# Kernel optimization log

Hardware: AMD Instinct MI355X
Metric: run time of the kernel (lower is better)

The kernel has to match this reference:

```python
import jax, jax.numpy as jnp
import numpy as np


def _lin(x, w, b):
    # torch Linear: y = x @ w.T + b, w shape [out, in]
    return x @ w.T + b


def setup_inputs() -> dict:
    key = jax.random.key(0)
    ks = jax.random.split(key, 24)
    D, L1, L2, L3, C = 784, 128, 64, 32, 10
    B = 65536
    s = 0.05
    inp = {
        'x': jax.random.normal(ks[0], (B, D), jnp.float32),
        'W1_w': jax.random.normal(ks[1], (L1, D), jnp.float32) * s,
        'W1_b': jnp.zeros((L1,), jnp.float32),
        'U1_w': jax.random.normal(ks[2], (L1, L1), jnp.float32) * s,
        'U1_b': jnp.zeros((L1,), jnp.float32),
        'W2_w': jax.random.normal(ks[3], (L2, L1), jnp.float32) * s,
        'W2_b': jnp.zeros((L2,), jnp.float32),
        'U2_w': jax.random.normal(ks[4], (L2, L2), jnp.float32) * s,
        'U2_b': jnp.zeros((L2,), jnp.float32),
        'W3_w': jax.random.normal(ks[5], (L3, L2), jnp.float32) * s,
        'W3_b': jnp.zeros((L3,), jnp.float32),
        'U3_w': jax.random.normal(ks[6], (L3, L3), jnp.float32) * s,
        'U3_b': jnp.zeros((L3,), jnp.float32),
        'fb3_w': jax.random.normal(ks[7], (L2, L3), jnp.float32) * s,
        'fb3_b': jnp.zeros((L2,), jnp.float32),
        'fb2_w': jax.random.normal(ks[8], (L1, L2), jnp.float32) * s,
        'fb2_b': jnp.zeros((L1,), jnp.float32),
        'fb1_w': jax.random.normal(ks[9], (D, L1), jnp.float32) * s,
        'fb1_b': jnp.zeros((D,), jnp.float32),
        'clf_w': jax.random.normal(ks[10], (C, L3), jnp.float32) * s,
        'clf_b': jnp.zeros((C,), jnp.float32),
        'steps': 5,
    }
    return inp


def reference(x, W1_w, W1_b, U1_w, U1_b, W2_w, W2_b, U2_w, U2_b,
              W3_w, W3_b, U3_w, U3_b, fb3_w, fb3_b, fb2_w, fb2_b,
              fb1_w, fb1_b, clf_w, clf_b, steps):
    B = x.shape[0]
    x = x.reshape(B, -1)
    h1 = jnp.zeros((B, W1_w.shape[0]), x.dtype)
    h2 = jnp.zeros((B, W2_w.shape[0]), x.dtype)
    h3 = jnp.zeros((B, W3_w.shape[0]), x.dtype)
    for _ in range(steps):  # fixed small step count (5)
        err_h2 = h2 - _lin(h3, fb3_w, fb3_b)
        err_h1 = h1 - _lin(h2, fb2_w, fb2_b)
        err_x = x - _lin(h1, fb1_w, fb1_b)
        h3 = h3 + jnp.tanh(_lin(err_h2, W3_w, W3_b)) + jnp.tanh(_lin(h3, U3_w, U3_b))
        h2 = h2 + jnp.tanh(_lin(err_h1, W2_w, W2_b)) + jnp.tanh(_lin(h2, U2_w, U2_b))
        h1 = h1 + jnp.tanh(_lin(err_x, W1_w, W1_b)) + jnp.tanh(_lin(h1, U1_w, U1_b))
    return _lin(h3, clf_w, clf_b)
```

## Files before the change

### kernel.cpp

```cpp
#include <hip/hip_runtime.h>
#include <stdint.h>

typedef __attribute__((ext_vector_type(8))) __bf16 bf16x8;
typedef __attribute__((ext_vector_type(8))) unsigned short u16x8;
typedef __attribute__((ext_vector_type(4))) unsigned short u16x4;
typedef __attribute__((ext_vector_type(4))) float f32x4;

#define WSF_M1 0
#define WSF_M2 16384
#define WSF_M3 20480
#define WSF_C  21504
#define F_W1T 0
#define F_M1N 102400
#define F_U1T 118784
#define F_W2T 135168
#define F_M2N 143360
#define F_U2T 147456
#define F_W3T 151552
#define F_M3N 153600
#define F_U3T 154624
#define F_CLF 155648

__device__ __forceinline__ unsigned short f2bf(float f) {
  uint32_t u = __builtin_bit_cast(uint32_t, f);
  u += 0x7fffu + ((u >> 16) & 1u);
  return (unsigned short)(u >> 16);
}

extern "C" __device__ float __ocml_native_exp2_f32(float);
__device__ __forceinline__ float tanh_fast(float x) {
  float e = __ocml_native_exp2_f32(x * 2.8853900817779268f);
  return 1.0f - 2.0f * __builtin_amdgcn_rcpf(e + 1.0f);
}

__device__ __forceinline__ f32x4 mfma16(bf16x8 a, bf16x8 b, f32x4 c) {
  return __builtin_amdgcn_mfma_f32_16x16x32_bf16(a, b, c, 0, 0, 0);
}

__device__ __forceinline__ bf16x8 lds_frag(const unsigned short* p) {
  u16x8 v = *(const u16x8*)p;
  return __builtin_bit_cast(bf16x8, v);
}
__device__ __forceinline__ bf16x8 glb_frag(const unsigned short* __restrict__ base,
                                           int fi, int lane) {
  u16x8 v = *(const u16x8*)(base + (((size_t)fi * 64 + lane) << 3));
  return __builtin_bit_cast(bf16x8, v);
}

__global__ __launch_bounds__(256)
void pcnet_prep(
    const float* __restrict__ W1_w, const float* __restrict__ W1_b,
    const float* __restrict__ W2_w, const float* __restrict__ W2_b,
    const float* __restrict__ W3_w, const float* __restrict__ W3_b,
    const float* __restrict__ fb1_w, const float* __restrict__ fb1_b,
    const float* __restrict__ fb2_w, const float* __restrict__ fb2_b,
    const float* __restrict__ fb3_w, const float* __restrict__ fb3_b,
    float* __restrict__ wsf)
{
  const int w    = blockIdx.x * 4 + (threadIdx.x >> 6);
  const int lane = threadIdx.x & 63;
  float s = 0.f;
  if (w < 16384) {
    const int a = w >> 7, b = w & 127;
    for (int d = lane; d < 784; d += 64) s += fb1_w[d*128 + a] * W1_w[b*784 + d];
  } else if (w < 20480) {
    const int t = w - 16384, a = t >> 6, b = t & 63;
    for (int d = lane; d < 128; d += 64) s += fb2_w[d*64 + a] * W2_w[b*128 + d];
  } else if (w < 21504) {
    const int t = w - 20480, a = t >> 5, b = t & 31;
    s = fb3_w[lane*32 + a] * W3_w[b*64 + lane];
  } else if (w < 21632) {
    const int b = w - 21504;
    for (int d = lane; d < 784; d += 64) s += fb1_b[d] * W1_w[b*784 + d];
  } else if (w < 21696) {
    const int b = w - 21632;
    for (int d = lane; d < 128; d += 64) s += fb2_b[d] * W2_w[b*128 + d];
  } else if (w < 21728) {
    const int b = w - 21696;
    s = fb3_b[lane] * W3_w[b*64 + lane];
  }
#pragma unroll
  for (int off = 32; off >= 1; off >>= 1) s += __shfl_down(s, off, 64);
  if (lane == 0) {
    if (w < 16384)      wsf[WSF_M1 + (w >> 7)*128 + (w & 127)] = -s;
    else if (w < 20480) { const int t = w - 16384; wsf[WSF_M2 + (t >> 6)*64 + (t & 63)] = -s; }
    else if (w < 21504) { const int t = w - 20480; wsf[WSF_M3 + (t >> 5)*32 + (t & 31)] = -s; }
    else if (w < 21632) { const int b = w - 21504; wsf[WSF_C + b]       = W1_b[b] - s; }
    else if (w < 21696) { const int b = w - 21632; wsf[WSF_C + 128 + b] = W2_b[b] - s; }
    else if (w < 21728) { const int b = w - 21696; wsf[WSF_C + 192 + b] = W3_b[b] - s; }
  }
}

__device__ __forceinline__ void swz_T(const float* __restrict__ src, int ld, int Kv, int Nv,
                                      int NT, unsigned short* __restrict__ dst, int f, int lane) {
  const int kt = f / NT, nt = f - kt*NT;
  const int m = lane & 15, q = lane >> 4;
  const int n = nt*16 + m;
  u16x8 v;
#pragma unroll
  for (int j = 0; j < 8; ++j) {
    const int k = kt*32 + q*8 + j;
    float val = (k < Kv && n < Nv) ? src[(size_t)n*ld + k] : 0.f;
    v[j] = f2bf(val);
  }
  *(u16x8*)(dst + (((size_t)f*64 + lane) << 3)) = v;
}
__device__ __forceinline__ void swz_R(const float* __restrict__ src, int N, int NT,
                                      unsigned short* __restrict__ dst, int f, int lane) {
  const int kt = f / NT, nt = f - kt*NT;
  const int m = lane & 15, q = lane >> 4;
  const int n = nt*16 + m;
  u16x8 v;
#pragma unroll
  for (int j = 0; j < 8; ++j) {
    const int k = kt*32 + q*8 + j;
    v[j] = f2bf(src[k*N + n]);
  }
  *(u16x8*)(dst + (((size_t)f*64 + lane) << 3)) = v;
}

__global__ void pcnet_swz(
    const float* __restrict__ W1_w, const float* __restrict__ U1_w,
    const float* __restrict__ W2_w, const float* __restrict__ U2_w,
    const float* __restrict__ W3_w, const float* __restrict__ U3_w,
    const float* __restrict__ clf_w, const float* __restrict__ wsf,
    unsigned short* __restrict__ frags)
{
  const int t = blockIdx.x*256 + threadIdx.x;
  if (t >= 305*64) return;
  const int fg = t >> 6, lane = t & 63;
  if      (fg < 200) swz_T(W1_w, 784, 784, 128, 8, frags + F_W1T, fg,       lane);
  else if (fg < 232) swz_R(wsf + WSF_M1, 128, 8,  frags + F_M1N, fg - 200, lane);
  else if (fg < 264) swz_T(U1_w, 128, 128, 128, 8, frags + F_U1T, fg - 232, lane);
  else if (fg < 280) swz_T(W2_w, 128, 128, 64, 4, frags + F_W2T, fg - 264, lane);
  else if (fg < 288) swz_R(wsf + WSF_M2, 64, 4,   frags + F_M2N, fg - 280, lane);
  else if (fg < 296) swz_T(U2_w, 64, 64, 64, 4,   frags + F_U2T, fg - 288, lane);
  else if (fg < 300) swz_T(W3_w, 64, 64, 32, 2,   frags + F_W3T, fg - 296, lane);
  else if (fg < 302) swz_R(wsf + WSF_M3, 32, 2,   frags + F_M3N, fg - 300, lane);
  else if (fg < 304) swz_T(U3_w, 32, 32, 32, 2,   frags + F_U3T, fg - 302, lane);
  else               swz_T(clf_w, 32, 32, 10, 1,  frags + F_CLF, fg - 304, lane);
}

__global__ __launch_bounds__(256, 2)
void pcnet_main(
    const float* __restrict__ x,
    const float* __restrict__ cvec,
    const float* __restrict__ U1_b, const float* __restrict__ U2_b,
    const float* __restrict__ U3_b, const float* __restrict__ clf_b,
    const unsigned short* __restrict__ frags,
    const int* __restrict__ steps_p,
    float* __restrict__ out)
{
  const int tid  = threadIdx.x;
  const int wave = tid >> 6;
  const int lane = tid & 63;
  const int q = lane >> 4;
  const int m = lane & 15;
  const int rowBase = blockIdx.x << 5;

  __shared__ unsigned short h1b[32*136];
  __shared__ unsigned short h2b[32*72];
  __shared__ unsigned short h3b[32*40];
  __shared__ unsigned short xst[2][32*40];

  const unsigned short* fW1T = frags + F_W1T;
  const unsigned short* fM1N = frags + F_M1N;
  const unsigned short* fU1T = frags + F_U1T;
  const unsigned short* fW2T = frags + F_W2T;
  const unsigned short* fM2N = frags + F_M2N;
  const unsigned short* fU2T = frags + F_U2T;
  const unsigned short* fW3T = frags + F_W3T;
  const unsigned short* fM3N = frags + F_M3N;
  const unsigned short* fU3T = frags + F_U3T;
  const unsigned short* fCLF = frags + F_CLF;

  f32x4 A1[2][2];
#pragma unroll
  for (int nt = 0; nt < 2; ++nt) {
    const float cv = cvec[(2*wave + nt)*16 + m];
    const f32x4 v = {cv, cv, cv, cv};
    A1[0][nt] = v; A1[1][nt] = v;
  }

  const int srow = tid >> 3;
  const int kq   = (tid & 7) << 2;
  const float* __restrict__ xrow = x + (size_t)(rowBase + srow)*784;

  {
    f32x4 va = *(const f32x4*)(xrow + kq);
    u16x4 pk;
    pk[0]=f2bf(va[0]); pk[1]=f2bf(va[1]); pk[2]=f2bf(va[2]); pk[3]=f2bf(va[3]);
    *(u16x4*)(xst[0] + srow*40 + kq) = pk;
  }

  for (int kt = 0; kt < 25; ++kt) {
    __syncthreads();
    if (kt < 24) {
      const int gk = (kt + 1)*32 + kq;
      f32x4 va = {0.f,0.f,0.f,0.f};
      if (gk < 784) va = *(const f32x4*)(xrow + gk);
      u16x4 pk;
      pk[0]=f2bf(va[0]); pk[1]=f2bf(va[1]); pk[2]=f2bf(va[2]); pk[3]=f2bf(va[3]);
      *(u16x4*)(xst[(kt+1)&1] + srow*40 + kq) = pk;
    }
    const unsigned short* xb = xst[kt & 1];
    const bf16x8 a0 = lds_frag(xb + (0*16 + m)*40 + q*8);
    const bf16x8 a1 = lds_frag(xb + (1*16 + m)*40 + q*8);
#pragma unroll
    for (int nt = 0; nt < 2; ++nt) {
      const bf16x8 b = glb_frag(fW1T, kt*8 + 2*wave + nt, lane);
      A1[0][nt] = mfma16(a0, b, A1[0][nt]);
      A1[1][nt] = mfma16(a1, b, A1[1][nt]);
    }
  }

  {
    uint32_t* p = (uint32_t*)h1b;
    for (int i = tid; i < 2176; i += 256) p[i] = 0u;
    p = (uint32_t*)h2b;
    for (int i = tid; i < 1152; i += 256) p[i] = 0u;
    p = (uint32_t*)h3b;
    for (int i = tid; i < 640; i += 256) p[i] = 0u;
  }
  f32x4 h1v[2][2], h2v[2], h3v;
  {
    const f32x4 z = {0.f,0.f,0.f,0.f};
#pragma unroll
    for (int rt = 0; rt < 2; ++rt) { h1v[rt][0] = z; h1v[rt][1] = z; h2v[rt] = z; }
    h3v = z;
  }

  const int nt3 = wave >> 1;
  const int rt3 = wave & 1;
  const float c3v  = cvec[192 + nt3*16 + m];
  const float b3v  = U3_b[nt3*16 + m];
  const float c2v  = cvec[128 + wave*16 + m];
  const float b2v  = U2_b[wave*16 + m];
  const float b1v0 = U1_b[(2*wave + 0)*16 + m];
  const float b1v1 = U1_b[(2*wave + 1)*16 + m];

  __syncthreads();

  const int S = *steps_p;
  for (int s = 0; s < S; ++s) {
    bf16x8 h2f[2][2];
#pragma unroll
    for (int kt = 0; kt < 2; ++kt)
#pragma unroll
      for (int rt = 0; rt < 2; ++rt)
        h2f[kt][rt] = lds_frag(h2b + (rt*16 + m)*72 + kt*32 + q*8);
    const bf16x8 h3f = lds_frag(h3b + (rt3*16 + m)*40 + q*8);
    bf16x8 h2s[2];
#pragma unroll
    for (int kt = 0; kt < 2; ++kt) h2s[kt] = (wave & 1) ? h2f[kt][1] : h2f[kt][0];

    f32x4 z3a = {c3v,c3v,c3v,c3v};
    f32x4 z3b = {b3v,b3v,b3v,b3v};
#pragma unroll
    for (int kt = 0; kt < 2; ++kt) {
      const bf16x8 b = glb_frag(fW3T, kt*2 + nt3, lane);
      z3a = mfma16(h2s[kt], b, z3a);
    }
    { const bf16x8 b = glb_frag(fM3N, nt3, lane); z3a = mfma16(h3f, b, z3a); }
    { const bf16x8 b = glb_frag(fU3T, nt3, lane); z3b = mfma16(h3f, b, z3b); }
#pragma unroll
    for (int r = 0; r < 4; ++r)
      h3v[r] += tanh_fast(z3a[r]) + tanh_fast(z3b[r]);

    f32x4 z2b[2];
    { const f32x4 v = {b2v,b2v,b2v,b2v}; z2b[0]=v; z2b[1]=v; }
#pragma unroll
    for (int kt = 0; kt < 2; ++kt) {
      const bf16x8 b = glb_frag(fU2T, kt*4 + wave, lane);
#pragma unroll
      for (int rt = 0; rt < 2; ++rt) z2b[rt] = mfma16(h2f[kt][rt], b, z2b[rt]);
    }
#pragma unroll
    for (int rt = 0; rt < 2; ++rt)
#pragma unroll
      for (int r = 0; r < 4; ++r) h2v[rt][r] += tanh_fast(z2b[rt][r]);

    f32x4 z2a[2];
    { const f32x4 v = {c2v,c2v,c2v,c2v}; z2a[0]=v; z2a[1]=v; }
#pragma unroll
    for (int kt = 0; kt < 2; ++kt) {
      const bf16x8 b = glb_frag(fM2N, kt*4 + wave, lane);
#pragma unroll
      for (int rt = 0; rt < 2; ++rt) z2a[rt] = mfma16(h2f[kt][rt], b, z2a[rt]);
    }

    f32x4 z1a[2][2], z1b[2][2];
    { const f32x4 v0 = {b1v0,b1v0,b1v0,b1v0};
      const f32x4 v1 = {b1v1,b1v1,b1v1,b1v1};
#pragma unroll
      for (int rt = 0; rt < 2; ++rt) {
        z1a[rt][0] = A1[rt][0]; z1a[rt][1] = A1[rt][1];
        z1b[rt][0] = v0;        z1b[rt][1] = v1;
      }
    }
#pragma unroll
    for (int kt = 0; kt < 4; ++kt) {
      const bf16x8 a0 = lds_frag(h1b + (0*16 + m)*136 + kt*32 + q*8);
      const bf16x8 a1 = lds_frag(h1b + (1*16 + m)*136 + kt*32 + q*8);
      const bf16x8 bW = glb_frag(fW2T, kt*4 + wave, lane);
      z2a[0] = mfma16(a0, bW, z2a[0]);
      z2a[1] = mfma16(a1, bW, z2a[1]);
      const bf16x8 bM0 = glb_frag(fM1N, kt*8 + 2*wave + 0, lane);
      const bf16x8 bM1 = glb_frag(fM1N, kt*8 + 2*wave + 1, lane);
      z1a[0][0] = mfma16(a0, bM0, z1a[0][0]); z1a[0][1] = mfma16(a0, bM1, z1a[0][1]);
      z1a[1][0] = mfma16(a1, bM0, z1a[1][0]); z1a[1][1] = mfma16(a1, bM1, z1a[1][1]);
      const bf16x8 bU0 = glb_frag(fU1T, kt*8 + 2*wave + 0, lane);
      const bf16x8 bU1 = glb_frag(fU1T, kt*8 + 2*wave + 1, lane);
      z1b[0][0] = mfma16(a0, bU0, z1b[0][0]); z1b[0][1] = mfma16(a0, bU1, z1b[0][1]);
      z1b[1][0] = mfma16(a1, bU0, z1b[1][0]); z1b[1][1] = mfma16(a1, bU1, z1b[1][1]);
    }
#pragma unroll
    for (int rt = 0; rt < 2; ++rt)
#pragma unroll
      for (int r = 0; r < 4; ++r) h2v[rt][r] += tanh_fast(z2a[rt][r]);
#pragma unroll
    for (int rt = 0; rt < 2; ++rt)
#pragma unroll
      for (int nt = 0; nt < 2; ++nt)
#pragma unroll
        for (int r = 0; r < 4; ++r)
          h1v[rt][nt][r] += tanh_fast(z1a[rt][nt][r]) + tanh_fast(z1b[rt][nt][r]);

    __syncthreads();
#pragma unroll
    for (int rt = 0; rt < 2; ++rt) {
#pragma unroll
      for (int nt = 0; nt < 2; ++nt)
#pragma unroll
        for (int r = 0; r < 4; ++r)
          h1b[(rt*16 + q*4 + r)*136 + (2*wave + nt)*16 + m] = f2bf(h1v[rt][nt][r]);
#pragma unroll
      for (int r = 0; r < 4; ++r)
        h2b[(rt*16 + q*4 + r)*72 + wave*16 + m] = f2bf(h2v[rt][r]);
    }
#pragma unroll
    for (int r = 0; r < 4; ++r)
      h3b[(rt3*16 + q*4 + r)*40 + nt3*16 + m] = f2bf(h3v[r]);
    __syncthreads();
  }

  if (wave < 2) {
    f32x4 o;
    { const float cb = (m < 10) ? clf_b[m] : 0.f; o = (f32x4){cb, cb, cb, cb}; }
    const bf16x8 a = lds_frag(h3b + (wave*16 + m)*40 + q*8);
    const bf16x8 b = glb_frag(fCLF, 0, lane);
    o = mfma16(a, b, o);
    if (m < 10) {
#pragma unroll
      for (int r = 0; r < 4; ++r) {
        const int row = rowBase + wave*16 + q*4 + r;
        out[(size_t)row*10 + m] = o[r];
      }
    }
  }
}

extern "C" void kernel_launch(void* const* d_in, const int* in_sizes, int n_in,
                              void* d_out, int out_size, void* d_ws, size_t ws_size,
                              hipStream_t stream)
{
  (void)in_sizes; (void)n_in; (void)out_size; (void)ws_size;
  const float* x     = (const float*)d_in[0];
  const float* W1_w  = (const float*)d_in[1];
  const float* W1_b  = (const float*)d_in[2];
  const float* U1_w  = (const float*)d_in[3];
  const float* U1_b  = (const float*)d_in[4];
  const float* W2_w  = (const float*)d_in[5];
  const float* W2_b  = (const float*)d_in[6];
  const float* U2_w  = (const float*)d_in[7];
  const float* U2_b  = (const float*)d_in[8];
  const float* W3_w  = (const float*)d_in[9];
  const float* W3_b  = (const float*)d_in[10];
  const float* U3_w  = (const float*)d_in[11];
  const float* U3_b  = (const float*)d_in[12];
  const float* fb3_w = (const float*)d_in[13];
  const float* fb3_b = (const float*)d_in[14];
  const float* fb2_w = (const float*)d_in[15];
  const float* fb2_b = (const float*)d_in[16];
  const float* fb1_w = (const float*)d_in[17];
  const float* fb1_b = (const float*)d_in[18];
  const float* clf_w = (const float*)d_in[19];
  const float* clf_b = (const float*)d_in[20];
  const int*   steps = (const int*)d_in[21];

  float* wsf = (float*)d_ws;
  unsigned short* frags = (unsigned short*)d_ws + 43520;

  hipLaunchKernelGGL(pcnet_prep, dim3(5432), dim3(256), 0, stream,
                     W1_w, W1_b, W2_w, W2_b, W3_w, W3_b,
                     fb1_w, fb1_b, fb2_w, fb2_b, fb3_w, fb3_b, wsf);
  hipLaunchKernelGGL(pcnet_swz, dim3(77), dim3(256), 0, stream,
                     W1_w, U1_w, W2_w, U2_w, W3_w, U3_w, clf_w, wsf, frags);
  hipLaunchKernelGGL(pcnet_main, dim3(2048), dim3(256), 0, stream,
                     x, wsf + WSF_C, U1_b, U2_b, U3_b, clf_b, frags, steps,
                     (float*)d_out);
}
```

Before: 480.5 us.

## Load x fragments directly from global, split M1 prep kernel, raise occupancy

```diff
diff --git a/kernel.cpp b/kernel.cpp
--- a/kernel.cpp
+++ b/kernel.cpp
@@ -3,7 +3,6 @@
 
 typedef __attribute__((ext_vector_type(8))) __bf16 bf16x8;
 typedef __attribute__((ext_vector_type(8))) unsigned short u16x8;
-typedef __attribute__((ext_vector_type(4))) unsigned short u16x4;
 typedef __attribute__((ext_vector_type(4))) float f32x4;
 
 #define WSF_M1 0
@@ -46,24 +45,44 @@
   u16x8 v = *(const u16x8*)(base + (((size_t)fi * 64 + lane) << 3));
   return __builtin_bit_cast(bf16x8, v);
 }
+__device__ __forceinline__ bf16x8 pack8(f32x4 a, f32x4 b) {
+  u16x8 v;
+  v[0]=f2bf(a[0]); v[1]=f2bf(a[1]); v[2]=f2bf(a[2]); v[3]=f2bf(a[3]);
+  v[4]=f2bf(b[0]); v[5]=f2bf(b[1]); v[6]=f2bf(b[2]); v[7]=f2bf(b[3]);
+  return __builtin_bit_cast(bf16x8, v);
+}
+
+__global__ __launch_bounds__(128)
+void pcnet_prep_m1(const float* __restrict__ W1_w, const float* __restrict__ fb1_w,
+                   float* __restrict__ wsf)
+{
+  const int b = blockIdx.x;
+  const int a = threadIdx.x;
+  const float* __restrict__ wr = W1_w + (size_t)b*784;
+  float s0=0.f, s1=0.f, s2=0.f, s3=0.f;
+  for (int d = 0; d < 784; d += 4) {
+    s0 += wr[d]   * fb1_w[(d  )*128 + a];
+    s1 += wr[d+1] * fb1_w[(d+1)*128 + a];
+    s2 += wr[d+2] * fb1_w[(d+2)*128 + a];
+    s3 += wr[d+3] * fb1_w[(d+3)*128 + a];
+  }
+  wsf[WSF_M1 + a*128 + b] = -((s0+s1)+(s2+s3));
+}
 
 __global__ __launch_bounds__(256)
-void pcnet_prep(
+void pcnet_prep_rest(
     const float* __restrict__ W1_w, const float* __restrict__ W1_b,
     const float* __restrict__ W2_w, const float* __restrict__ W2_b,
     const float* __restrict__ W3_w, const float* __restrict__ W3_b,
-    const float* __restrict__ fb1_w, const float* __restrict__ fb1_b,
+    const float* __restrict__ fb1_b,
     const float* __restrict__ fb2_w, const float* __restrict__ fb2_b,
     const float* __restrict__ fb3_w, const float* __restrict__ fb3_b,
     float* __restrict__ wsf)
 {
-  const int w    = blockIdx.x * 4 + (threadIdx.x >> 6);
+  const int w    = 16384 + blockIdx.x * 4 + (threadIdx.x >> 6);
   const int lane = threadIdx.x & 63;
   float s = 0.f;
-  if (w < 16384) {
-    const int a = w >> 7, b = w & 127;
-    for (int d = lane; d < 784; d += 64) s += fb1_w[d*128 + a] * W1_w[b*784 + d];
-  } else if (w < 20480) {
+  if (w < 20480) {
     const int t = w - 16384, a = t >> 6, b = t & 63;
     for (int d = lane; d < 128; d += 64) s += fb2_w[d*64 + a] * W2_w[b*128 + d];
   } else if (w < 21504) {
@@ -82,8 +101,7 @@
 #pragma unroll
   for (int off = 32; off >= 1; off >>= 1) s += __shfl_down(s, off, 64);
   if (lane == 0) {
-    if (w < 16384)      wsf[WSF_M1 + (w >> 7)*128 + (w & 127)] = -s;
-    else if (w < 20480) { const int t = w - 16384; wsf[WSF_M2 + (t >> 6)*64 + (t & 63)] = -s; }
+    if (w < 20480)      { const int t = w - 16384; wsf[WSF_M2 + (t >> 6)*64 + (t & 63)] = -s; }
     else if (w < 21504) { const int t = w - 20480; wsf[WSF_M3 + (t >> 5)*32 + (t & 31)] = -s; }
     else if (w < 21632) { const int b = w - 21504; wsf[WSF_C + b]       = W1_b[b] - s; }
     else if (w < 21696) { const int b = w - 21632; wsf[WSF_C + 128 + b] = W2_b[b] - s; }
@@ -141,7 +159,7 @@
   else               swz_T(clf_w, 32, 32, 10, 1,  frags + F_CLF, fg - 304, lane);
 }
 
-__global__ __launch_bounds__(256, 2)
+__global__ __launch_bounds__(256, 3)
 void pcnet_main(
     const float* __restrict__ x,
     const float* __restrict__ cvec,
@@ -161,7 +179,6 @@
   __shared__ unsigned short h1b[32*136];
   __shared__ unsigned short h2b[32*72];
   __shared__ unsigned short h3b[32*40];
-  __shared__ unsigned short xst[2][32*40];
 
   const unsigned short* fW1T = frags + F_W1T;
   const unsigned short* fM1N = frags + F_M1N;
@@ -174,46 +191,6 @@
   const unsigned short* fU3T = frags + F_U3T;
   const unsigned short* fCLF = frags + F_CLF;
 
-  f32x4 A1[2][2];
-#pragma unroll
-  for (int nt = 0; nt < 2; ++nt) {
-    const float cv = cvec[(2*wave + nt)*16 + m];
-    const f32x4 v = {cv, cv, cv, cv};
-    A1[0][nt] = v; A1[1][nt] = v;
-  }
-
-  const int srow = tid >> 3;
-  const int kq   = (tid & 7) << 2;
-  const float* __restrict__ xrow = x + (size_t)(rowBase + srow)*784;
-
-  {
-    f32x4 va = *(const f32x4*)(xrow + kq);
-    u16x4 pk;
-    pk[0]=f2bf(va[0]); pk[1]=f2bf(va[1]); pk[2]=f2bf(va[2]); pk[3]=f2bf(va[3]);
-    *(u16x4*)(xst[0] + srow*40 + kq) = pk;
-  }
-
-  for (int kt = 0; kt < 25; ++kt) {
-    __syncthreads();
-    if (kt < 24) {
-      const int gk = (kt + 1)*32 + kq;
-      f32x4 va = {0.f,0.f,0.f,0.f};
-      if (gk < 784) va = *(const f32x4*)(xrow + gk);
-      u16x4 pk;
-      pk[0]=f2bf(va[0]); pk[1]=f2bf(va[1]); pk[2]=f2bf(va[2]); pk[3]=f2bf(va[3]);
-      *(u16x4*)(xst[(kt+1)&1] + srow*40 + kq) = pk;
-    }
-    const unsigned short* xb = xst[kt & 1];
-    const bf16x8 a0 = lds_frag(xb + (0*16 + m)*40 + q*8);
-    const bf16x8 a1 = lds_frag(xb + (1*16 + m)*40 + q*8);
-#pragma unroll
-    for (int nt = 0; nt < 2; ++nt) {
-      const bf16x8 b = glb_frag(fW1T, kt*8 + 2*wave + nt, lane);
-      A1[0][nt] = mfma16(a0, b, A1[0][nt]);
-      A1[1][nt] = mfma16(a1, b, A1[1][nt]);
-    }
-  }
-
   {
     uint32_t* p = (uint32_t*)h1b;
     for (int i = tid; i < 2176; i += 256) p[i] = 0u;
@@ -222,6 +199,51 @@
     p = (uint32_t*)h3b;
     for (int i = tid; i < 640; i += 256) p[i] = 0u;
   }
+
+  f32x4 A1[2][2];
+#pragma unroll
+  for (int nt = 0; nt < 2; ++nt) {
+    const float cv = cvec[(2*wave + nt)*16 + m];
+    const f32x4 v = {cv, cv, cv, cv};
+    A1[0][nt] = v; A1[1][nt] = v;
+  }
+
+  const float* __restrict__ xr0 = x + (size_t)(rowBase + m)*784      + q*8;
+  const float* __restrict__ xr1 = x + (size_t)(rowBase + 16 + m)*784 + q*8;
+
+#pragma unroll 4
+  for (int kt = 0; kt < 24; ++kt) {
+    const f32x4 p0 = *(const f32x4*)(xr0 + kt*32);
+    const f32x4 p1 = *(const f32x4*)(xr0 + kt*32 + 4);
+    const f32x4 p2 = *(const f32x4*)(xr1 + kt*32);
+    const f32x4 p3 = *(const f32x4*)(xr1 + kt*32 + 4);
+    const bf16x8 a0 = pack8(p0, p1);
+    const bf16x8 a1 = pack8(p2, p3);
+#pragma unroll
+    for (int nt = 0; nt < 2; ++nt) {
+      const bf16x8 b = glb_frag(fW1T, kt*8 + 2*wave + nt, lane);
+      A1[0][nt] = mfma16(a0, b, A1[0][nt]);
+      A1[1][nt] = mfma16(a1, b, A1[1][nt]);
+    }
+  }
+  {
+    f32x4 p0 = {0,0,0,0}, p1 = p0, p2 = p0, p3 = p0;
+    if (q < 2) {
+      p0 = *(const f32x4*)(xr0 + 768);
+      p1 = *(const f32x4*)(xr0 + 772);
+      p2 = *(const f32x4*)(xr1 + 768);
+      p3 = *(const f32x4*)(xr1 + 772);
+    }
+    const bf16x8 a0 = pack8(p0, p1);
+    const bf16x8 a1 = pack8(p2, p3);
+#pragma unroll
+    for (int nt = 0; nt < 2; ++nt) {
+      const bf16x8 b = glb_frag(fW1T, 24*8 + 2*wave + nt, lane);
+      A1[0][nt] = mfma16(a0, b, A1[0][nt]);
+      A1[1][nt] = mfma16(a1, b, A1[1][nt]);
+    }
+  }
+
   f32x4 h1v[2][2], h2v[2], h3v;
   {
     const f32x4 z = {0.f,0.f,0.f,0.f};
@@ -254,77 +276,103 @@
 #pragma unroll
     for (int kt = 0; kt < 2; ++kt) h2s[kt] = (wave & 1) ? h2f[kt][1] : h2f[kt][0];
 
-    f32x4 z3a = {c3v,c3v,c3v,c3v};
-    f32x4 z3b = {b3v,b3v,b3v,b3v};
-#pragma unroll
-    for (int kt = 0; kt < 2; ++kt) {
-      const bf16x8 b = glb_frag(fW3T, kt*2 + nt3, lane);
-      z3a = mfma16(h2s[kt], b, z3a);
-    }
-    { const bf16x8 b = glb_frag(fM3N, nt3, lane); z3a = mfma16(h3f, b, z3a); }
-    { const bf16x8 b = glb_frag(fU3T, nt3, lane); z3b = mfma16(h3f, b, z3b); }
-#pragma unroll
-    for (int r = 0; r < 4; ++r)
-      h3v[r] += tanh_fast(z3a[r]) + tanh_fast(z3b[r]);
-
-    f32x4 z2b[2];
-    { const f32x4 v = {b2v,b2v,b2v,b2v}; z2b[0]=v; z2b[1]=v; }
-#pragma unroll
-    for (int kt = 0; kt < 2; ++kt) {
-      const bf16x8 b = glb_frag(fU2T, kt*4 + wave, lane);
-#pragma unroll
-      for (int rt = 0; rt < 2; ++rt) z2b[rt] = mfma16(h2f[kt][rt], b, z2b[rt]);
-    }
-#pragma unroll
-    for (int rt = 0; rt < 2; ++rt)
-#pragma unroll
-      for (int r = 0; r < 4; ++r) h2v[rt][r] += tanh_fast(z2b[rt][r]);
-
-    f32x4 z2a[2];
-    { const f32x4 v = {c2v,c2v,c2v,c2v}; z2a[0]=v; z2a[1]=v; }
-#pragma unroll
-    for (int kt = 0; kt < 2; ++kt) {
-      const bf16x8 b = glb_frag(fM2N, kt*4 + wave, lane);
-#pragma unroll
-      for (int rt = 0; rt < 2; ++rt) z2a[rt] = mfma16(h2f[kt][rt], b, z2a[rt]);
-    }
-
-    f32x4 z1a[2][2], z1b[2][2];
-    { const f32x4 v0 = {b1v0,b1v0,b1v0,b1v0};
-      const f32x4 v1 = {b1v1,b1v1,b1v1,b1v1};
-#pragma unroll
-      for (int rt = 0; rt < 2; ++rt) {
-        z1a[rt][0] = A1[rt][0]; z1a[rt][1] = A1[rt][1];
-        z1b[rt][0] = v0;        z1b[rt][1] = v1;
-      }
-    }
-#pragma unroll
-    for (int kt = 0; kt < 4; ++kt) {
-      const bf16x8 a0 = lds_frag(h1b + (0*16 + m)*136 + kt*32 + q*8);
-      const bf16x8 a1 = lds_frag(h1b + (1*16 + m)*136 + kt*32 + q*8);
-      const bf16x8 bW = glb_frag(fW2T, kt*4 + wave, lane);
-      z2a[0] = mfma16(a0, bW, z2a[0]);
-      z2a[1] = mfma16(a1, bW, z2a[1]);
-      const bf16x8 bM0 = glb_frag(fM1N, kt*8 + 2*wave + 0, lane);
-      const bf16x8 bM1 = glb_frag(fM1N, kt*8 + 2*wave + 1, lane);
-      z1a[0][0] = mfma16(a0, bM0, z1a[0][0]); z1a[0][1] = mfma16(a0, bM1, z1a[0][1]);
-      z1a[1][0] = mfma16(a1, bM0, z1a[1][0]); z1a[1][1] = mfma16(a1, bM1, z1a[1][1]);
-      const bf16x8 bU0 = glb_frag(fU1T, kt*8 + 2*wave + 0, lane);
-      const bf16x8 bU1 = glb_frag(fU1T, kt*8 + 2*wave + 1, lane);
-      z1b[0][0] = mfma16(a0, bU0, z1b[0][0]); z1b[0][1] = mfma16(a0, bU1, z1b[0][1]);
-      z1b[1][0] = mfma16(a1, bU0, z1b[1][0]); z1b[1][1] = mfma16(a1, bU1, z1b[1][1]);
-    }
-#pragma unroll
-    for (int rt = 0; rt < 2; ++rt)
-#pragma unroll
-      for (int r = 0; r < 4; ++r) h2v[rt][r] += tanh_fast(z2a[rt][r]);
-#pragma unroll
-    for (int rt = 0; rt < 2; ++rt)
-#pragma unroll
-      for (int nt = 0; nt < 2; ++nt)
-#pragma unroll
-        for (int r = 0; r < 4; ++r)
-          h1v[rt][nt][r] += tanh_fast(z1a[rt][nt][r]) + tanh_fast(z1b[rt][nt][r]);
+    {
+      f32x4 z3a = {c3v,c3v,c3v,c3v};
+      f32x4 z3b = {b3v,b3v,b3v,b3v};
+#pragma unroll
+      for (int kt = 0; kt < 2; ++kt) {
+        const bf16x8 b = glb_frag(fW3T, kt*2 + nt3, lane);
+        z3a = mfma16(h2s[kt], b, z3a);
+      }
+      { const bf16x8 b = glb_frag(fM3N, nt3, lane); z3a = mfma16(h3f, b, z3a); }
+      { const bf16x8 b = glb_frag(fU3T, nt3, lane); z3b = mfma16(h3f, b, z3b); }
+#pragma unroll
+      for (int r = 0; r < 4; ++r)
+        h3v[r] += tanh_fast(z3a[r]) + tanh_fast(z3b[r]);
+    }
+
+    {
+      f32x4 z2b[2];
+      { const f32x4 v = {b2v,b2v,b2v,b2v}; z2b[0]=v; z2b[1]=v; }
+#pragma unroll
+      for (int kt = 0; kt < 2; ++kt) {
+        const bf16x8 b = glb_frag(fU2T, kt*4 + wave, lane);
+#pragma unroll
+        for (int rt = 0; rt < 2; ++rt) z2b[rt] = mfma16(h2f[kt][rt], b, z2b[rt]);
+      }
+#pragma unroll
+      for (int rt = 0; rt < 2; ++rt)
+#pragma unroll
+        for (int r = 0; r < 4; ++r) h2v[rt][r] += tanh_fast(z2b[rt][r]);
+    }
+
+    {
+      f32x4 z2a[2];
+      { const f32x4 v = {c2v,c2v,c2v,c2v}; z2a[0]=v; z2a[1]=v; }
+#pragma unroll
+      for (int kt = 0; kt < 2; ++kt) {
+        const bf16x8 b = glb_frag(fM2N, kt*4 + wave, lane);
+#pragma unroll
+        for (int rt = 0; rt < 2; ++rt) z2a[rt] = mfma16(h2f[kt][rt], b, z2a[rt]);
+      }
+#pragma unroll
+      for (int kt = 0; kt < 4; ++kt) {
+        const bf16x8 a0 = lds_frag(h1b + (0*16 + m)*136 + kt*32 + q*8);
+        const bf16x8 a1 = lds_frag(h1b + (1*16 + m)*136 + kt*32 + q*8);
+        const bf16x8 b  = glb_frag(fW2T, kt*4 + wave, lane);
+        z2a[0] = mfma16(a0, b, z2a[0]);
+        z2a[1] = mfma16(a1, b, z2a[1]);
+      }
+#pragma unroll
+      for (int rt = 0; rt < 2; ++rt)
+#pragma unroll
+        for (int r = 0; r < 4; ++r) h2v[rt][r] += tanh_fast(z2a[rt][r]);
+    }
+
+    {
+      f32x4 z1[2][2];
+#pragma unroll
+      for (int rt = 0; rt < 2; ++rt) { z1[rt][0] = A1[rt][0]; z1[rt][1] = A1[rt][1]; }
+#pragma unroll
+      for (int kt = 0; kt < 4; ++kt) {
+        const bf16x8 a0 = lds_frag(h1b + (0*16 + m)*136 + kt*32 + q*8);
+        const bf16x8 a1 = lds_frag(h1b + (1*16 + m)*136 + kt*32 + q*8);
+        const bf16x8 b0 = glb_frag(fM1N, kt*8 + 2*wave + 0, lane);
+        const bf16x8 b1 = glb_frag(fM1N, kt*8 + 2*wave + 1, lane);
+        z1[0][0] = mfma16(a0, b0, z1[0][0]); z1[0][1] = mfma16(a0, b1, z1[0][1]);
+        z1[1][0] = mfma16(a1, b0, z1[1][0]); z1[1][1] = mfma16(a1, b1, z1[1][1]);
+      }
+#pragma unroll
+      for (int rt = 0; rt < 2; ++rt)
+#pragma unroll
+        for (int nt = 0; nt < 2; ++nt)
+#pragma unroll
+          for (int r = 0; r < 4; ++r) h1v[rt][nt][r] += tanh_fast(z1[rt][nt][r]);
+    }
+
+    {
+      f32x4 z1[2][2];
+      { const f32x4 v0 = {b1v0,b1v0,b1v0,b1v0};
+        const f32x4 v1 = {b1v1,b1v1,b1v1,b1v1};
+#pragma unroll
+        for (int rt = 0; rt < 2; ++rt) { z1[rt][0] = v0; z1[rt][1] = v1; }
+      }
+#pragma unroll
+      for (int kt = 0; kt < 4; ++kt) {
+        const bf16x8 a0 = lds_frag(h1b + (0*16 + m)*136 + kt*32 + q*8);
+        const bf16x8 a1 = lds_frag(h1b + (1*16 + m)*136 + kt*32 + q*8);
+        const bf16x8 b0 = glb_frag(fU1T, kt*8 + 2*wave + 0, lane);
+        const bf16x8 b1 = glb_frag(fU1T, kt*8 + 2*wave + 1, lane);
+        z1[0][0] = mfma16(a0, b0, z1[0][0]); z1[0][1] = mfma16(a0, b1, z1[0][1]);
+        z1[1][0] = mfma16(a1, b0, z1[1][0]); z1[1][1] = mfma16(a1, b1, z1[1][1]);
+      }
+#pragma unroll
+      for (int rt = 0; rt < 2; ++rt)
+#pragma unroll
+        for (int nt = 0; nt < 2; ++nt)
+#pragma unroll
+          for (int r = 0; r < 4; ++r) h1v[rt][nt][r] += tanh_fast(z1[rt][nt][r]);
+    }
 
     __syncthreads();
 #pragma unroll
@@ -391,9 +439,11 @@
   float* wsf = (float*)d_ws;
   unsigned short* frags = (unsigned short*)d_ws + 43520;
 
-  hipLaunchKernelGGL(pcnet_prep, dim3(5432), dim3(256), 0, stream,
+  hipLaunchKernelGGL(pcnet_prep_m1, dim3(128), dim3(128), 0, stream,
+                     W1_w, fb1_w, wsf);
+  hipLaunchKernelGGL(pcnet_prep_rest, dim3(1336), dim3(256), 0, stream,
                      W1_w, W1_b, W2_w, W2_b, W3_w, W3_b,
-                     fb1_w, fb1_b, fb2_w, fb2_b, fb3_w, fb3_b, wsf);
+                     fb1_b, fb2_w, fb2_b, fb3_w, fb3_b, wsf);
   hipLaunchKernelGGL(pcnet_swz, dim3(77), dim3(256), 0, stream,
                      W1_w, U1_w, W2_w, U2_w, W3_w, U3_w, clf_w, wsf, frags);
   hipLaunchKernelGGL(pcnet_main, dim3(2048), dim3(256), 0, stream,
```

New measurement: 618.2 us. 1.29x slower.
